# Kernel tuning notes

Hardware: AMD Instinct MI355X
Metric: run time of the kernel (lower is better)

The kernel has to match this reference:

```python
import jax, jax.numpy as jnp
import numpy as np

HIDDEN = 512
LAYERS = 2
MAX_ROLLOUT = 12
STATE_SIZE = [8, 6, 4, 1]
ANCHOR = 64
BATCH = 1024
BLOCK_N = len(STATE_SIZE)


def setup_inputs() -> dict:
    key = jax.random.key(0)
    ks = jax.random.split(key, 20)
    s = 0.05
    d = {}
    d["x0"] = jax.random.normal(ks[0], (1, BATCH, HIDDEN), jnp.float32)
    d["lstm_Wih"] = jax.random.normal(ks[1], (LAYERS, 4 * HIDDEN, HIDDEN), jnp.float32) * s
    d["lstm_Whh"] = jax.random.normal(ks[2], (LAYERS, 4 * HIDDEN, HIDDEN), jnp.float32) * s
    d["lstm_bih"] = jax.random.normal(ks[3], (LAYERS, 4 * HIDDEN), jnp.float32) * s
    d["lstm_bhh"] = jax.random.normal(ks[4], (LAYERS, 4 * HIDDEN), jnp.float32) * s
    d["Wc0"] = jax.random.normal(ks[5], (STATE_SIZE[0], HIDDEN), jnp.float32) * s
    d["bc0"] = jax.random.normal(ks[6], (STATE_SIZE[0],), jnp.float32) * s
    d["Wc1"] = jax.random.normal(ks[7], (STATE_SIZE[1], HIDDEN), jnp.float32) * s
    d["bc1"] = jax.random.normal(ks[8], (STATE_SIZE[1],), jnp.float32) * s
    d["Wc2"] = jax.random.normal(ks[9], (STATE_SIZE[2], HIDDEN), jnp.float32) * s
    d["bc2"] = jax.random.normal(ks[10], (STATE_SIZE[2],), jnp.float32) * s
    d["Wprev"] = jax.random.normal(ks[11], (ANCHOR, HIDDEN), jnp.float32) * s
    d["bprev"] = jax.random.normal(ks[12], (ANCHOR,), jnp.float32) * s
    d["Wcurr"] = jax.random.normal(ks[13], (ANCHOR, HIDDEN), jnp.float32) * s
    d["bcurr"] = jax.random.normal(ks[14], (ANCHOR,), jnp.float32) * s
    d["Wanc"] = jax.random.normal(ks[15], (HIDDEN, MAX_ROLLOUT - 1), jnp.float32) * s
    d["banc"] = jax.random.normal(ks[16], (HIDDEN,), jnp.float32) * s
    d["v"] = jax.random.normal(ks[17], (ANCHOR,), jnp.float32)
    d["batch_size"] = BATCH
    return d


def _lstm_step(x, h, c, Wih, Whh, bih, bhh):
    # x: [B,H]; h,c: [L,B,H]; multi-layer LSTM, torch gate order (i,f,g,o)
    hs, cs = [], []
    inp = x
    for l in range(LAYERS):
        g = inp @ Wih[l].T + h[l] @ Whh[l].T + bih[l] + bhh[l]  # [B,4H]
        gi, gf, gg, go = jnp.split(g, 4, axis=-1)
        cl = jax.nn.sigmoid(gf) * c[l] + jax.nn.sigmoid(gi) * jnp.tanh(gg)
        hl = jax.nn.sigmoid(go) * jnp.tanh(cl)
        hs.append(hl)
        cs.append(cl)
        inp = hl
    return inp, jnp.stack(hs), jnp.stack(cs)


def _forward(x0, lstm_Wih, lstm_Whh, lstm_bih, lstm_bhh, Wc0, bc0, Wc1, bc1, Wc2, bc2,
             Wprev, bprev, Wcurr, bcurr, Wanc, banc, v, batch_size):
    Wcls = [Wc0, Wc1, Wc2]
    bcls = [bc0, bc1, bc2]
    B = batch_size
    anchor_hs = [jnp.zeros((B, HIDDEN), x0.dtype)]
    inp = x0[0]  # [B,H]
    h = jnp.zeros((LAYERS, B, HIDDEN), x0.dtype)
    c = jnp.zeros((LAYERS, B, HIDDEN), x0.dtype)
    outputs = []
    for i in range(MAX_ROLLOUT * BLOCK_N):
        state_idx = i % BLOCK_N
        cycle_idx = i // BLOCK_N
        out, h, c = _lstm_step(inp, h, c, lstm_Wih, lstm_Whh, lstm_bih, lstm_bhh)
        if state_idx < BLOCK_N - 1:
            logit = out @ Wcls[state_idx].T + bcls[state_idx]
            outputs.append(jax.nn.softmax(logit, axis=-1))  # [B, STATE_SIZE[state_idx]]
            # note: `inp` is NOT updated on classifier steps, matching the original
        else:
            anchor_hs.append(out)
            if cycle_idx == 0:
                anchor_o = jnp.zeros((B, MAX_ROLLOUT - 1), x0.dtype)
            else:
                # attention over anchor_hs[0:cycle_idx] (zeros + previous cycles),
                # exactly as the original indexes after appending current out
                prev = jnp.stack(anchor_hs[:cycle_idx])  # [cyc, B, H]
                t = jnp.tanh(prev @ Wprev.T + bprev + (out @ Wcurr.T + bcurr)[None])  # [cyc,B,A]
                scores = jax.nn.sigmoid(jnp.einsum('a,cba->cb', v, t))  # [cyc, B]
                anchor_o = jnp.pad(scores.T, ((0, 0), (0, MAX_ROLLOUT - cycle_idx - 1)))
            outputs.append(anchor_o)  # [B, MAX_ROLLOUT-1]
            inp = anchor_o @ Wanc.T + banc  # anchor_embedding feeds next step
    # outputs are [B, S_i] / [B, MAX_ROLLOUT-1]; concat into a single [B, 348] tensor
    return jnp.concatenate(outputs, axis=1)


def reference(x0, lstm_Wih, lstm_Whh, lstm_bih, lstm_bhh, Wc0, bc0, Wc1, bc1, Wc2, bc2,
              Wprev, bprev, Wcurr, bcurr, Wanc, banc, v, batch_size):
    return _forward(x0, lstm_Wih, lstm_Whh, lstm_bih, lstm_bhh, Wc0, bc0, Wc1, bc1, Wc2, bc2,
                    Wprev, bprev, Wcurr, bcurr, Wanc, banc, v, batch_size)
```

## Files before the change

### kernel.cpp

```cpp
#include <hip/hip_runtime.h>
#include <hip/hip_bf16.h>

#define BATCH 1024
#define HID   512
#define OUTW  348

using short8 = __attribute__((ext_vector_type(8))) short;
using bf16x8 = __attribute__((ext_vector_type(8))) __bf16;
using f32x4  = __attribute__((ext_vector_type(4))) float;

__device__ __forceinline__ float bf2f(unsigned short u) {
  union { unsigned int i; float f; } x; x.i = ((unsigned int)u) << 16; return x.f;
}
__device__ __forceinline__ unsigned short f2bf(float f) {
  __hip_bfloat16 b = __float2bfloat16(f);
  return __builtin_bit_cast(unsigned short, b);
}
__device__ __forceinline__ float sigm(float x) { return 1.0f / (1.0f + __expf(-x)); }

__device__ __forceinline__ f32x4 mfma_bf16(short8 a, short8 b, f32x4 c) {
  return __builtin_amdgcn_mfma_f32_16x16x32_bf16(
      __builtin_bit_cast(bf16x8, a), __builtin_bit_cast(bf16x8, b), c, 0, 0, 0);
}

typedef const __attribute__((address_space(1))) unsigned int* gas_p;
typedef __attribute__((address_space(3))) unsigned int* las_p;
__device__ __forceinline__ void gload16(const void* g, void* l) {
  __builtin_amdgcn_global_load_lds((gas_p)g, (las_p)l, 16, 0, 0);
}


__global__ void k_convert(const float* __restrict__ src, unsigned short* __restrict__ dst, int n) {
  int i = (blockIdx.x * blockDim.x + threadIdx.x) * 4;
  if (i + 3 < n) {
    float4 v = *(const float4*)(src + i);
    dst[i + 0] = f2bf(v.x); dst[i + 1] = f2bf(v.y);
    dst[i + 2] = f2bf(v.z); dst[i + 3] = f2bf(v.w);
  } else {
    for (int j = 0; j < 4 && i + j < n; ++j) dst[i + j] = f2bf(src[i + j]);
  }
}

__global__ void k_wqp(const float* __restrict__ Wcurr, const float* __restrict__ Wprev,
                      unsigned short* __restrict__ dst) {
  int i = blockIdx.x * blockDim.x + threadIdx.x;
  int row = i >> 9, col = i & 511;
  float v = (row < 64) ? Wcurr[row * 512 + col] : Wprev[(row - 64) * 512 + col];
  dst[i] = f2bf(v);
}

__global__ void k_bias(const float* __restrict__ bih, const float* __restrict__ bhh,
                       float* __restrict__ bsum) {
  int i = blockIdx.x * blockDim.x + threadIdx.x;
  if (i < 4096) bsum[i] = bih[i] + bhh[i];
}

__global__ void k_zero(uint4* __restrict__ p, int n16) {
  int i = blockIdx.x * blockDim.x + threadIdx.x;
  if (i < n16) p[i] = make_uint4(0u, 0u, 0u, 0u);
}

__global__ void k_p0(float* __restrict__ P, const float* __restrict__ bprev) {
  int i = blockIdx.x * blockDim.x + threadIdx.x;
  P[i] = bprev[i & 63];
}


struct GJob {
  const unsigned short *X, *H, *Wih, *Whh;
  const float *bias;
  float *C;
  unsigned short *Hout;
};
struct CJob {
  const unsigned short* h;
  const float *Wc, *bc;
  float* out;
  int obase;
};

__device__ __forceinline__ void run_gemm(const GJob& j, int lb,
                                         unsigned short (*Ab)[4096],
                                         unsigned short (*Bb)[4096]) {
  const int w = threadIdx.x >> 6, lane = threadIdx.x & 63;
  const int mt = lb >> 5;
  const int nt = (lb & 7) * 4 + ((lb >> 3) & 3);
  const int m0 = mt * 64;
  const int n0 = nt * 16;
  const int l16 = lane & 15, kg = lane >> 4;

  auto stage = [&](int kt, int buf) {
    const unsigned short* Asrc = (kt < 8) ? j.X : j.H;
    const unsigned short* Wsrc = (kt < 8) ? j.Wih : j.Whh;
    const int k0 = (kt & 7) * 64;
#pragma unroll
    for (int i = 0; i < 2; ++i) {
      int s = w * 128 + i * 64 + lane;
      int row = s >> 3;
      int ke = ((s & 7) ^ (row & 7)) << 3;
      gload16(Asrc + (size_t)(m0 + row) * HID + k0 + ke, &Ab[buf][(w * 128 + i * 64) * 8]);
    }
#pragma unroll
    for (int i = 0; i < 2; ++i) {
      int s = w * 128 + i * 64 + lane;
      int fr = s >> 3;
      int g = fr >> 4, c = fr & 15;
      int ke = ((s & 7) ^ (fr & 7)) << 3;
      gload16(Wsrc + (size_t)(g * 512 + n0 + c) * HID + k0 + ke, &Bb[buf][(w * 128 + i * 64) * 8]);
    }
  };

  f32x4 acc[4];
#pragma unroll
  for (int g = 0; g < 4; ++g) acc[g] = (f32x4)(0.0f);

  stage(0, 0);
  for (int kt = 0; kt < 16; ++kt) {
    __syncthreads();
    if (kt < 15) stage(kt + 1, (kt + 1) & 1);
    const int buf = kt & 1;
#pragma unroll
    for (int ko = 0; ko < 2; ++ko) {
      const int acb = ko * 64 + kg * 16;
      const int ar = w * 16 + l16;
      short8 a = *(const short8*)&Ab[buf][ar * 64 + ((acb ^ ((ar & 7) << 4)) >> 1)];
#pragma unroll
      for (int g = 0; g < 4; ++g) {
        const int br = g * 16 + l16;
        short8 b = *(const short8*)&Bb[buf][br * 64 + ((acb ^ ((br & 7) << 4)) >> 1)];
        acc[g] = mfma_bf16(a, b, acc[g]);
      }
    }
  }

  const int ccol = n0 + l16;
  const int crow = m0 + w * 16 + kg * 4;
  const float b0 = j.bias[ccol], b1 = j.bias[512 + ccol];
  const float b2 = j.bias[1024 + ccol], b3 = j.bias[1536 + ccol];
#pragma unroll
  for (int r = 0; r < 4; ++r) {
    const int m = crow + r;
    float gi = acc[0][r] + b0;
    float gf = acc[1][r] + b1;
    float gg = acc[2][r] + b2;
    float go = acc[3][r] + b3;
    float cold = j.C[m * HID + ccol];
    float cn = sigm(gf) * cold + sigm(gi) * tanhf(gg);
    float hn = sigm(go) * tanhf(cn);
    j.C[m * HID + ccol] = cn;
    j.Hout[m * HID + ccol] = f2bf(hn);
  }
}

template <int S>
__device__ __forceinline__ void run_cls(const CJob& c, int cb) {
  const int w = threadIdx.x >> 6, lane = threadIdx.x & 63;
#pragma unroll
  for (int i = 0; i < 8; ++i) {
    const int r = (cb * 4 + w) * 8 + i;
    short8 hv = *(const short8*)(c.h + r * HID + lane * 8);
    float hf[8];
#pragma unroll
    for (int j = 0; j < 8; ++j) hf[j] = bf2f((unsigned short)hv[j]);
    float logit[S];
#pragma unroll
    for (int s = 0; s < S; ++s) {
      const float* wr = c.Wc + s * HID + lane * 8;
      float p = 0.f;
#pragma unroll
      for (int j = 0; j < 8; ++j) p += hf[j] * wr[j];
#pragma unroll
      for (int off = 32; off; off >>= 1) p += __shfl_xor(p, off);
      logit[s] = p + c.bc[s];
    }
    if (lane == 0) {
      float m = logit[0];
#pragma unroll
      for (int s = 1; s < S; ++s) m = fmaxf(m, logit[s]);
      float e[S], den = 0.f;
#pragma unroll
      for (int s = 0; s < S; ++s) { e[s] = __expf(logit[s] - m); den += e[s]; }
      float inv = 1.0f / den;
#pragma unroll
      for (int s = 0; s < S; ++s) c.out[r * OUTW + c.obase + s] = e[s] * inv;
    }
  }
}

template <int S>
__global__ __launch_bounds__(256, 4) void k_gates1(GJob A, CJob C) {
  __shared__ unsigned short Ab[2][4096];
  __shared__ unsigned short Bb[2][4096];
  const int b = blockIdx.x;
  if (b < 512) {
    run_gemm(A, b, Ab, Bb);
  } else {
    if constexpr (S > 0) run_cls<S>(C, b - 512);
  }
}

__global__ __launch_bounds__(256) void k_qp(
    const unsigned short* __restrict__ h1,
    const unsigned short* __restrict__ Wqp,
    const float* __restrict__ bcurr, const float* __restrict__ bprev,
    float* __restrict__ Q,
    float* __restrict__ P,
    int cyc) {
  __shared__ unsigned short Ab[2][4096];
  __shared__ unsigned short Bb[2][1024];
  const int w = threadIdx.x >> 6, lane = threadIdx.x & 63;
  const int m0 = blockIdx.x * 64, n0 = blockIdx.y * 16;
  const int l16 = lane & 15, kg = lane >> 4;

  auto stage = [&](int kt, int buf) {
    const int k0 = kt * 64;
#pragma unroll
    for (int j = 0; j < 2; ++j) {
      int s = w * 128 + j * 64 + lane;
      int row = s >> 3;
      int ke = ((s & 7) ^ (row & 7)) << 3;
      gload16(h1 + (size_t)(m0 + row) * HID + k0 + ke, &Ab[buf][(w * 128 + j * 64) * 8]);
    }
    if (w < 2) {
      int s = w * 64 + lane;
      int row = s >> 3;
      int ke = ((s & 7) ^ (row & 7)) << 3;
      gload16(Wqp + (size_t)(n0 + row) * HID + k0 + ke, &Bb[buf][(w * 64) * 8]);
    }
  };

  f32x4 acc = (f32x4)(0.0f);
  stage(0, 0);
  for (int kt = 0; kt < 8; ++kt) {
    __syncthreads();
    if (kt < 7) stage(kt + 1, (kt + 1) & 1);
    const int buf = kt & 1;
#pragma unroll
    for (int ko = 0; ko < 2; ++ko) {
      const int acb = ko * 64 + kg * 16;
      const int ar = w * 16 + l16;
      short8 a = *(const short8*)&Ab[buf][ar * 64 + ((acb ^ ((ar & 7) << 4)) >> 1)];
      const int br = l16;
      short8 b = *(const short8*)&Bb[buf][br * 64 + ((acb ^ ((br & 7) << 4)) >> 1)];
      acc = mfma_bf16(a, b, acc);
    }
  }

  const int col = n0 + l16;
  const int r0 = m0 + w * 16 + kg * 4;
#pragma unroll
  for (int r = 0; r < 4; ++r) {
    const int m = r0 + r;
    float val = acc[r] + (col < 64 ? bcurr[col] : bprev[col - 64]);
    if (col < 64) Q[m * 64 + col] = val;
    else if (cyc + 1 < 12) P[(cyc + 1) * (BATCH * 64) + m * 64 + (col - 64)] = val;
  }
}

template <int CYC>
__global__ __launch_bounds__(256) void k_scores(
    const float* __restrict__ Q, const float* __restrict__ P,
    const float* __restrict__ vv, const float* __restrict__ Wanc,
    const float* __restrict__ banc, float* __restrict__ out,
    unsigned short* __restrict__ X) {
  const int w = threadIdx.x >> 6, lane = threadIdx.x & 63;
  const int r = blockIdx.x * 4 + w;
  const float q = Q[r * 64 + lane];
  const float vl = vv[lane];
  float sk[CYC > 0 ? CYC : 1];
#pragma unroll
  for (int k = 0; k < CYC; ++k) {
    float t = tanhf(P[k * (BATCH * 64) + r * 64 + lane] + q) * vl;
#pragma unroll
    for (int off = 32; off; off >>= 1) t += __shfl_xor(t, off);
    sk[k] = sigm(t);
  }
  float ov = 0.0f;
#pragma unroll
  for (int k = 0; k < 11; ++k)
    if (lane == k) ov = (k < CYC) ? sk[k] : 0.0f;
  if (lane < 11) out[r * OUTW + CYC * 29 + 18 + lane] = ov;

  const int d0 = lane * 8;
#pragma unroll
  for (int j = 0; j < 8; ++j) {
    const int d = d0 + j;
    float x = banc[d];
#pragma unroll
    for (int k = 0; k < CYC; ++k) x += sk[k] * Wanc[d * 11 + k];
    X[r * HID + d] = f2bf(x);
  }
}


extern "C" void kernel_launch(void* const* d_in, const int* in_sizes, int n_in,
                              void* d_out, int out_size, void* d_ws, size_t ws_size,
                              hipStream_t stream) {
  const float* x0    = (const float*)d_in[0];
  const float* lWih  = (const float*)d_in[1];
  const float* lWhh  = (const float*)d_in[2];
  const float* lbih  = (const float*)d_in[3];
  const float* lbhh  = (const float*)d_in[4];
  const float* Wc0   = (const float*)d_in[5];
  const float* bc0   = (const float*)d_in[6];
  const float* Wc1   = (const float*)d_in[7];
  const float* bc1   = (const float*)d_in[8];
  const float* Wc2   = (const float*)d_in[9];
  const float* bc2   = (const float*)d_in[10];
  const float* Wprev = (const float*)d_in[11];
  const float* bprev = (const float*)d_in[12];
  const float* Wcurr = (const float*)d_in[13];
  const float* bcurr = (const float*)d_in[14];
  const float* Wanc  = (const float*)d_in[15];
  const float* banc  = (const float*)d_in[16];
  const float* v     = (const float*)d_in[17];
  float* out = (float*)d_out;

  const size_t NW  = 2 * 2048 * 512;
  const size_t NBH = (size_t)BATCH * HID;

  char* ws = (char*)d_ws;
  size_t off = 0;
  auto alloc = [&](size_t bytes) { char* p = ws + off; off += (bytes + 255) & ~(size_t)255; return p; };
  unsigned short* Wih_b = (unsigned short*)alloc(NW * 2);
  unsigned short* Whh_b = (unsigned short*)alloc(NW * 2);
  unsigned short* Wqp_b = (unsigned short*)alloc(128 * 512 * 2);
  float*          biasS = (float*)alloc(4096 * 4);
  unsigned short* Xb    = (unsigned short*)alloc(NBH * 2);
  unsigned short* Hb0   = (unsigned short*)alloc(2 * NBH * 2);
  unsigned short* Hb1   = (unsigned short*)alloc(2 * NBH * 2);
  float*          C0    = (float*)alloc(NBH * 4);
  float*          C1    = (float*)alloc(NBH * 4);
  float*          P     = (float*)alloc((size_t)12 * BATCH * 64 * 4);
  float*          Qb    = (float*)alloc((size_t)BATCH * 64 * 4);

  k_convert<<<dim3((NW / 4 + 255) / 256), dim3(256), 0, stream>>>(lWih, Wih_b, (int)NW);
  k_convert<<<dim3((NW / 4 + 255) / 256), dim3(256), 0, stream>>>(lWhh, Whh_b, (int)NW);
  k_convert<<<dim3((NBH / 4 + 255) / 256), dim3(256), 0, stream>>>(x0, Xb, (int)NBH);
  k_wqp<<<dim3(256), dim3(256), 0, stream>>>(Wcurr, Wprev, Wqp_b);
  k_bias<<<dim3(16), dim3(256), 0, stream>>>(lbih, lbhh, biasS);
  {
    size_t zb = 2 * NBH * 2 + 2 * NBH * 2 + NBH * 4 + NBH * 4;
    int n16 = (int)(zb / 16);
    k_zero<<<dim3((n16 + 255) / 256), dim3(256), 0, stream>>>((uint4*)Hb0, n16);
  }
  k_p0<<<dim3(256), dim3(256), 0, stream>>>(P, bprev);

  auto jobL0 = [&](int u) {
    GJob j; j.X = Xb; j.H = Hb0 + (u & 1) * NBH;
    j.Wih = Wih_b; j.Whh = Whh_b; j.bias = biasS; j.C = C0;
    j.Hout = Hb0 + ((u + 1) & 1) * NBH; return j;
  };
  auto jobL1 = [&](int t) {
    GJob j; j.X = Hb0 + ((t + 1) & 1) * NBH; j.H = Hb1 + (t & 1) * NBH;
    j.Wih = Wih_b + 2048 * 512; j.Whh = Whh_b + 2048 * 512; j.bias = biasS + 2048; j.C = C1;
    j.Hout = Hb1 + ((t + 1) & 1) * NBH; return j;
  };
  auto h1of = [&](int t) { return (const unsigned short*)(Hb1 + ((t + 1) & 1) * NBH); };
  CJob nocls{};

  k_gates1<0><<<dim3(512), dim3(256), 0, stream>>>(jobL0(0), nocls);

  for (int c = 0; c < 12; ++c) {
    const int t0 = 4 * c, t1 = t0 + 1, t2 = t0 + 2, t3 = t0 + 3;
    const int base = c * 29;
    CJob cls0{h1of(t0), Wc0, bc0, out, base};
    CJob cls1{h1of(t1), Wc1, bc1, out, base + 8};
    CJob cls2{h1of(t2), Wc2, bc2, out, base + 14};

    k_gates1<0><<<dim3(512), dim3(256), 0, stream>>>(jobL1(t0), nocls);
    k_gates1<0><<<dim3(512), dim3(256), 0, stream>>>(jobL0(t1), nocls);
    k_gates1<8><<<dim3(544), dim3(256), 0, stream>>>(jobL1(t1), cls0);
    k_gates1<0><<<dim3(512), dim3(256), 0, stream>>>(jobL0(t2), nocls);
    k_gates1<6><<<dim3(544), dim3(256), 0, stream>>>(jobL1(t2), cls1);
    k_gates1<0><<<dim3(512), dim3(256), 0, stream>>>(jobL0(t3), nocls);
    k_gates1<4><<<dim3(544), dim3(256), 0, stream>>>(jobL1(t3), cls2);

    k_qp<<<dim3(16, 8), dim3(256), 0, stream>>>(h1of(t3), Wqp_b, bcurr, bprev, Qb, P, c);
    switch (c) {
      case 0:  k_scores<0><<<dim3(256), dim3(256), 0, stream>>>(Qb, P, v, Wanc, banc, out, Xb); break;
      case 1:  k_scores<1><<<dim3(256), dim3(256), 0, stream>>>(Qb, P, v, Wanc, banc, out, Xb); break;
      case 2:  k_scores<2><<<dim3(256), dim3(256), 0, stream>>>(Qb, P, v, Wanc, banc, out, Xb); break;
      case 3:  k_scores<3><<<dim3(256), dim3(256), 0, stream>>>(Qb, P, v, Wanc, banc, out, Xb); break;
      case 4:  k_scores<4><<<dim3(256), dim3(256), 0, stream>>>(Qb, P, v, Wanc, banc, out, Xb); break;
      case 5:  k_scores<5><<<dim3(256), dim3(256), 0, stream>>>(Qb, P, v, Wanc, banc, out, Xb); break;
      case 6:  k_scores<6><<<dim3(256), dim3(256), 0, stream>>>(Qb, P, v, Wanc, banc, out, Xb); break;
      case 7:  k_scores<7><<<dim3(256), dim3(256), 0, stream>>>(Qb, P, v, Wanc, banc, out, Xb); break;
      case 8:  k_scores<8><<<dim3(256), dim3(256), 0, stream>>>(Qb, P, v, Wanc, banc, out, Xb); break;
      case 9:  k_scores<9><<<dim3(256), dim3(256), 0, stream>>>(Qb, P, v, Wanc, banc, out, Xb); break;
      case 10: k_scores<10><<<dim3(256), dim3(256), 0, stream>>>(Qb, P, v, Wanc, banc, out, Xb); break;
      default: k_scores<11><<<dim3(256), dim3(256), 0, stream>>>(Qb, P, v, Wanc, banc, out, Xb); break;
    }
    if (c < 11)
      k_gates1<0><<<dim3(512), dim3(256), 0, stream>>>(jobL0(t3 + 1), nocls);
  }
  (void)in_sizes; (void)n_in; (void)out_size; (void)ws_size;
}
```

Before: 1.994 ms.

## Halve LSTM GEMM M-tile, interleave gate rows, fuse anchor projection and scoring

The LSTM gate GEMM now uses 32-row M tiles with a 2x2 wave layout and doubles the grid to 1024 blocks. Weight rows are interleaved per cell so that a 16-column MFMA tile holds all four gates, and lane shuffles gather the gates for the cell update. The double-buffer sync is replaced by explicit vmcnt/lgkmcnt waits plus raw barriers. The separate Q/P projection and scoring kernels are fused into one per-16-row kernel that keeps Q in shared memory, which removes a launch and the Q global round trip. The trade-offs are more redundant weight loads per block, shuffle overhead in the epilogue, and only 64 blocks for the fused anchor kernel.

```diff
diff --git a/kernel.cpp b/kernel.cpp
--- a/kernel.cpp
+++ b/kernel.cpp
@@ -80,12 +80,13 @@
 };
 
 __device__ __forceinline__ void run_gemm(const GJob& j, int lb,
-                                         unsigned short (*Ab)[4096],
+                                         unsigned short (*Ab)[2048],
                                          unsigned short (*Bb)[4096]) {
-  const int w = threadIdx.x >> 6, lane = threadIdx.x & 63;
+  const int tid = threadIdx.x, w = tid >> 6, lane = tid & 63;
+  const int wm = w & 1, wn = w >> 1;
   const int mt = lb >> 5;
   const int nt = (lb & 7) * 4 + ((lb >> 3) & 3);
-  const int m0 = mt * 64;
+  const int m0 = mt * 32;
   const int n0 = nt * 16;
   const int l16 = lane & 15, kg = lane >> 4;
 
@@ -93,62 +94,73 @@
     const unsigned short* Asrc = (kt < 8) ? j.X : j.H;
     const unsigned short* Wsrc = (kt < 8) ? j.Wih : j.Whh;
     const int k0 = (kt & 7) * 64;
+    {
+      int s = tid, row = s >> 3;
+      int ke = ((s & 7) ^ (row & 7)) << 3;
+      gload16(Asrc + (size_t)(m0 + row) * HID + k0 + ke, &Ab[buf][s * 8]);
+    }
 #pragma unroll
     for (int i = 0; i < 2; ++i) {
-      int s = w * 128 + i * 64 + lane;
-      int row = s >> 3;
-      int ke = ((s & 7) ^ (row & 7)) << 3;
-      gload16(Asrc + (size_t)(m0 + row) * HID + k0 + ke, &Ab[buf][(w * 128 + i * 64) * 8]);
-    }
-#pragma unroll
-    for (int i = 0; i < 2; ++i) {
-      int s = w * 128 + i * 64 + lane;
-      int fr = s >> 3;
-      int g = fr >> 4, c = fr & 15;
-      int ke = ((s & 7) ^ (fr & 7)) << 3;
-      gload16(Wsrc + (size_t)(g * 512 + n0 + c) * HID + k0 + ke, &Bb[buf][(w * 128 + i * 64) * 8]);
+      int s = i * 256 + tid;
+      int gr = s >> 3;
+      int cell = gr >> 2, g = gr & 3;
+      int ke = ((s & 7) ^ (gr & 7)) << 3;
+      gload16(Wsrc + (size_t)(g * HID + n0 + cell) * HID + k0 + ke, &Bb[buf][s * 8]);
     }
   };
 
-  f32x4 acc[4];
-#pragma unroll
-  for (int g = 0; g < 4; ++g) acc[g] = (f32x4)(0.0f);
+  f32x4 acc[2];
+  acc[0] = (f32x4)(0.0f); acc[1] = (f32x4)(0.0f);
 
   stage(0, 0);
   for (int kt = 0; kt < 16; ++kt) {
-    __syncthreads();
-    if (kt < 15) stage(kt + 1, (kt + 1) & 1);
+    asm volatile("s_waitcnt lgkmcnt(0)" ::: "memory");
+    __builtin_amdgcn_s_barrier();
+    if (kt < 15) {
+      stage(kt + 1, (kt + 1) & 1);
+      asm volatile("s_waitcnt vmcnt(3)" ::: "memory");
+    } else {
+      asm volatile("s_waitcnt vmcnt(0)" ::: "memory");
+    }
+    __builtin_amdgcn_s_barrier();
+    __builtin_amdgcn_sched_barrier(0);
     const int buf = kt & 1;
+    const int ar = wm * 16 + l16;
+    const char* abase = (const char*)&Ab[buf][0] + ar * 128;
+    const char* bbase = (const char*)&Bb[buf][0];
 #pragma unroll
     for (int ko = 0; ko < 2; ++ko) {
-      const int acb = ko * 64 + kg * 16;
-      const int ar = w * 16 + l16;
-      short8 a = *(const short8*)&Ab[buf][ar * 64 + ((acb ^ ((ar & 7) << 4)) >> 1)];
-#pragma unroll
-      for (int g = 0; g < 4; ++g) {
-        const int br = g * 16 + l16;
-        short8 b = *(const short8*)&Bb[buf][br * 64 + ((acb ^ ((br & 7) << 4)) >> 1)];
-        acc[g] = mfma_bf16(a, b, acc[g]);
+      const int kb = ko * 64 + kg * 16;
+      short8 a = *(const short8*)(abase + (kb ^ ((ar & 7) << 4)));
+#pragma unroll
+      for (int t = 0; t < 2; ++t) {
+        const int br = wn * 32 + t * 16 + l16;
+        short8 b = *(const short8*)(bbase + br * 128 + (kb ^ ((br & 7) << 4)));
+        acc[t] = mfma_bf16(a, b, acc[t]);
       }
     }
   }
 
-  const int ccol = n0 + l16;
-  const int crow = m0 + w * 16 + kg * 4;
-  const float b0 = j.bias[ccol], b1 = j.bias[512 + ccol];
-  const float b2 = j.bias[1024 + ccol], b3 = j.bias[1536 + ccol];
-#pragma unroll
-  for (int r = 0; r < 4; ++r) {
-    const int m = crow + r;
-    float gi = acc[0][r] + b0;
-    float gf = acc[1][r] + b1;
-    float gg = acc[2][r] + b2;
-    float go = acc[3][r] + b3;
-    float cold = j.C[m * HID + ccol];
-    float cn = sigm(gf) * cold + sigm(gi) * tanhf(gg);
-    float hn = sigm(go) * tanhf(cn);
-    j.C[m * HID + ccol] = cn;
-    j.Hout[m * HID + ccol] = f2bf(hn);
+  const int g = l16 & 3;
+#pragma unroll
+  for (int t = 0; t < 2; ++t) {
+    const int cell = n0 + wn * 8 + t * 4 + (l16 >> 2);
+    const float bs = j.bias[g * HID + cell];
+#pragma unroll
+    for (int r = 0; r < 4; ++r) {
+      float val = acc[t][r] + bs;
+      float gf = __shfl(val, (lane & ~3) + 1);
+      float gg = __shfl(val, (lane & ~3) + 2);
+      float go = __shfl(val, (lane & ~3) + 3);
+      if (g == 0) {
+        const int m = m0 + wm * 16 + kg * 4 + r;
+        float cold = j.C[m * HID + cell];
+        float cn = sigm(gf) * cold + sigm(val) * tanhf(gg);
+        float hn = sigm(go) * tanhf(cn);
+        j.C[m * HID + cell] = cn;
+        j.Hout[m * HID + cell] = f2bf(hn);
+      }
+    }
   }
 }
 
@@ -189,47 +201,49 @@
 
 template <int S>
 __global__ __launch_bounds__(256, 4) void k_gates1(GJob A, CJob C) {
-  __shared__ unsigned short Ab[2][4096];
+  __shared__ unsigned short Ab[2][2048];
   __shared__ unsigned short Bb[2][4096];
   const int b = blockIdx.x;
-  if (b < 512) {
+  if (b < 1024) {
     run_gemm(A, b, Ab, Bb);
   } else {
-    if constexpr (S > 0) run_cls<S>(C, b - 512);
-  }
-}
-
-__global__ __launch_bounds__(256) void k_qp(
+    if constexpr (S > 0) run_cls<S>(C, b - 1024);
+  }
+}
+
+__global__ __launch_bounds__(256) void k_anchor2(
     const unsigned short* __restrict__ h1,
     const unsigned short* __restrict__ Wqp,
     const float* __restrict__ bcurr, const float* __restrict__ bprev,
-    float* __restrict__ Q,
-    float* __restrict__ P,
-    int cyc) {
-  __shared__ unsigned short Ab[2][4096];
-  __shared__ unsigned short Bb[2][1024];
-  const int w = threadIdx.x >> 6, lane = threadIdx.x & 63;
-  const int m0 = blockIdx.x * 64, n0 = blockIdx.y * 16;
+    const float* __restrict__ vv, const float* __restrict__ Wanc,
+    const float* __restrict__ banc,
+    float* __restrict__ P, float* __restrict__ out,
+    unsigned short* __restrict__ X, int cyc) {
+  __shared__ unsigned short Ab[2][1024];
+  __shared__ unsigned short Bb[2][8192];
+  __shared__ float Qs[16][64];
+  __shared__ float ss[16][12];
+  const int tid = threadIdx.x, w = tid >> 6, lane = tid & 63;
   const int l16 = lane & 15, kg = lane >> 4;
+  const int m0 = blockIdx.x * 16;
 
   auto stage = [&](int kt, int buf) {
     const int k0 = kt * 64;
-#pragma unroll
-    for (int j = 0; j < 2; ++j) {
-      int s = w * 128 + j * 64 + lane;
-      int row = s >> 3;
+    if (tid < 128) {
+      int s = tid, row = s >> 3;
       int ke = ((s & 7) ^ (row & 7)) << 3;
-      gload16(h1 + (size_t)(m0 + row) * HID + k0 + ke, &Ab[buf][(w * 128 + j * 64) * 8]);
-    }
-    if (w < 2) {
-      int s = w * 64 + lane;
-      int row = s >> 3;
+      gload16(h1 + (size_t)(m0 + row) * HID + k0 + ke, &Ab[buf][s * 8]);
+    }
+#pragma unroll
+    for (int i = 0; i < 4; ++i) {
+      int s = i * 256 + tid, row = s >> 3;
       int ke = ((s & 7) ^ (row & 7)) << 3;
-      gload16(Wqp + (size_t)(n0 + row) * HID + k0 + ke, &Bb[buf][(w * 64) * 8]);
+      gload16(Wqp + (size_t)row * HID + k0 + ke, &Bb[buf][s * 8]);
     }
   };
 
-  f32x4 acc = (f32x4)(0.0f);
+  f32x4 acc[2];
+  acc[0] = (f32x4)(0.0f); acc[1] = (f32x4)(0.0f);
   stage(0, 0);
   for (int kt = 0; kt < 8; ++kt) {
     __syncthreads();
@@ -237,58 +251,55 @@
     const int buf = kt & 1;
 #pragma unroll
     for (int ko = 0; ko < 2; ++ko) {
-      const int acb = ko * 64 + kg * 16;
-      const int ar = w * 16 + l16;
-      short8 a = *(const short8*)&Ab[buf][ar * 64 + ((acb ^ ((ar & 7) << 4)) >> 1)];
-      const int br = l16;
-      short8 b = *(const short8*)&Bb[buf][br * 64 + ((acb ^ ((br & 7) << 4)) >> 1)];
-      acc = mfma_bf16(a, b, acc);
-    }
-  }
-
-  const int col = n0 + l16;
-  const int r0 = m0 + w * 16 + kg * 4;
-#pragma unroll
-  for (int r = 0; r < 4; ++r) {
-    const int m = r0 + r;
-    float val = acc[r] + (col < 64 ? bcurr[col] : bprev[col - 64]);
-    if (col < 64) Q[m * 64 + col] = val;
-    else if (cyc + 1 < 12) P[(cyc + 1) * (BATCH * 64) + m * 64 + (col - 64)] = val;
-  }
-}
-
-template <int CYC>
-__global__ __launch_bounds__(256) void k_scores(
-    const float* __restrict__ Q, const float* __restrict__ P,
-    const float* __restrict__ vv, const float* __restrict__ Wanc,
-    const float* __restrict__ banc, float* __restrict__ out,
-    unsigned short* __restrict__ X) {
-  const int w = threadIdx.x >> 6, lane = threadIdx.x & 63;
-  const int r = blockIdx.x * 4 + w;
-  const float q = Q[r * 64 + lane];
-  const float vl = vv[lane];
-  float sk[CYC > 0 ? CYC : 1];
-#pragma unroll
-  for (int k = 0; k < CYC; ++k) {
-    float t = tanhf(P[k * (BATCH * 64) + r * 64 + lane] + q) * vl;
-#pragma unroll
-    for (int off = 32; off; off >>= 1) t += __shfl_xor(t, off);
-    sk[k] = sigm(t);
-  }
-  float ov = 0.0f;
-#pragma unroll
-  for (int k = 0; k < 11; ++k)
-    if (lane == k) ov = (k < CYC) ? sk[k] : 0.0f;
-  if (lane < 11) out[r * OUTW + CYC * 29 + 18 + lane] = ov;
-
-  const int d0 = lane * 8;
-#pragma unroll
-  for (int j = 0; j < 8; ++j) {
-    const int d = d0 + j;
-    float x = banc[d];
-#pragma unroll
-    for (int k = 0; k < CYC; ++k) x += sk[k] * Wanc[d * 11 + k];
-    X[r * HID + d] = f2bf(x);
+      const int kb = ko * 64 + kg * 16;
+      const int ar = l16;
+      short8 a = *(const short8*)((const char*)&Ab[buf][0] + ar * 128 + (kb ^ ((ar & 7) << 4)));
+#pragma unroll
+      for (int t = 0; t < 2; ++t) {
+        const int br = w * 32 + t * 16 + l16;
+        short8 b = *(const short8*)((const char*)&Bb[buf][0] + br * 128 + (kb ^ ((br & 7) << 4)));
+        acc[t] = mfma_bf16(a, b, acc[t]);
+      }
+    }
+  }
+
+#pragma unroll
+  for (int t = 0; t < 2; ++t) {
+    const int col = w * 32 + t * 16 + l16;
+#pragma unroll
+    for (int r = 0; r < 4; ++r) {
+      const int lr = kg * 4 + r;
+      float val = acc[t][r] + (col < 64 ? bcurr[col] : bprev[col - 64]);
+      if (col < 64) Qs[lr][col] = val;
+      else if (cyc + 1 < 12) P[(size_t)(cyc + 1) * (BATCH * 64) + (m0 + lr) * 64 + (col - 64)] = val;
+    }
+  }
+  __syncthreads();
+
+  for (int rr = 0; rr < 4; ++rr) {
+    const int lr = w * 4 + rr;
+    const float q = Qs[lr][lane];
+    float skv = 0.f;
+    for (int k = 0; k < cyc; ++k) {
+      float tt = tanhf(P[(size_t)k * (BATCH * 64) + (m0 + lr) * 64 + lane] + q) * vv[lane];
+#pragma unroll
+      for (int off = 32; off; off >>= 1) tt += __shfl_xor(tt, off);
+      float sk = sigm(tt);
+      if (lane == k) skv = sk;
+      if (lane == 0) ss[lr][k] = sk;
+    }
+    if (lane < 11) out[(size_t)(m0 + lr) * OUTW + cyc * 29 + 18 + lane] = (lane < cyc) ? skv : 0.f;
+  }
+  __syncthreads();
+
+  {
+    const int row = tid >> 4, dseg = tid & 15;
+    for (int jj = 0; jj < 32; ++jj) {
+      const int d = dseg * 32 + jj;
+      float x = banc[d];
+      for (int k = 0; k < cyc; ++k) x += ss[row][k] * Wanc[d * 11 + k];
+      X[(size_t)(m0 + row) * HID + d] = f2bf(x);
+    }
   }
 }
 
@@ -332,7 +343,6 @@
   float*          C0    = (float*)alloc(NBH * 4);
   float*          C1    = (float*)alloc(NBH * 4);
   float*          P     = (float*)alloc((size_t)12 * BATCH * 64 * 4);
-  float*          Qb    = (float*)alloc((size_t)BATCH * 64 * 4);
 
   k_convert<<<dim3((NW / 4 + 255) / 256), dim3(256), 0, stream>>>(lWih, Wih_b, (int)NW);
   k_convert<<<dim3((NW / 4 + 255) / 256), dim3(256), 0, stream>>>(lWhh, Whh_b, (int)NW);
@@ -359,7 +369,7 @@
   auto h1of = [&](int t) { return (const unsigned short*)(Hb1 + ((t + 1) & 1) * NBH); };
   CJob nocls{};
 
-  k_gates1<0><<<dim3(512), dim3(256), 0, stream>>>(jobL0(0), nocls);
+  k_gates1<0><<<dim3(1024), dim3(256), 0, stream>>>(jobL0(0), nocls);
 
   for (int c = 0; c < 12; ++c) {
     const int t0 = 4 * c, t1 = t0 + 1, t2 = t0 + 2, t3 = t0 + 3;
@@ -368,31 +378,18 @@
     CJob cls1{h1of(t1), Wc1, bc1, out, base + 8};
     CJob cls2{h1of(t2), Wc2, bc2, out, base + 14};
 
-    k_gates1<0><<<dim3(512), dim3(256), 0, stream>>>(jobL1(t0), nocls);
-    k_gates1<0><<<dim3(512), dim3(256), 0, stream>>>(jobL0(t1), nocls);
-    k_gates1<8><<<dim3(544), dim3(256), 0, stream>>>(jobL1(t1), cls0);
-    k_gates1<0><<<dim3(512), dim3(256), 0, stream>>>(jobL0(t2), nocls);
-    k_gates1<6><<<dim3(544), dim3(256), 0, stream>>>(jobL1(t2), cls1);
-    k_gates1<0><<<dim3(512), dim3(256), 0, stream>>>(jobL0(t3), nocls);
-    k_gates1<4><<<dim3(544), dim3(256), 0, stream>>>(jobL1(t3), cls2);
-
-    k_qp<<<dim3(16, 8), dim3(256), 0, stream>>>(h1of(t3), Wqp_b, bcurr, bprev, Qb, P, c);
-    switch (c) {
-      case 0:  k_scores<0><<<dim3(256), dim3(256), 0, stream>>>(Qb, P, v, Wanc, banc, out, Xb); break;
-      case 1:  k_scores<1><<<dim3(256), dim3(256), 0, stream>>>(Qb, P, v, Wanc, banc, out, Xb); break;
-      case 2:  k_scores<2><<<dim3(256), dim3(256), 0, stream>>>(Qb, P, v, Wanc, banc, out, Xb); break;
-      case 3:  k_scores<3><<<dim3(256), dim3(256), 0, stream>>>(Qb, P, v, Wanc, banc, out, Xb); break;
-      case 4:  k_scores<4><<<dim3(256), dim3(256), 0, stream>>>(Qb, P, v, Wanc, banc, out, Xb); break;
-      case 5:  k_scores<5><<<dim3(256), dim3(256), 0, stream>>>(Qb, P, v, Wanc, banc, out, Xb); break;
-      case 6:  k_scores<6><<<dim3(256), dim3(256), 0, stream>>>(Qb, P, v, Wanc, banc, out, Xb); break;
-      case 7:  k_scores<7><<<dim3(256), dim3(256), 0, stream>>>(Qb, P, v, Wanc, banc, out, Xb); break;
-      case 8:  k_scores<8><<<dim3(256), dim3(256), 0, stream>>>(Qb, P, v, Wanc, banc, out, Xb); break;
-      case 9:  k_scores<9><<<dim3(256), dim3(256), 0, stream>>>(Qb, P, v, Wanc, banc, out, Xb); break;
-      case 10: k_scores<10><<<dim3(256), dim3(256), 0, stream>>>(Qb, P, v, Wanc, banc, out, Xb); break;
-      default: k_scores<11><<<dim3(256), dim3(256), 0, stream>>>(Qb, P, v, Wanc, banc, out, Xb); break;
-    }
+    k_gates1<0><<<dim3(1024), dim3(256), 0, stream>>>(jobL1(t0), nocls);
+    k_gates1<0><<<dim3(1024), dim3(256), 0, stream>>>(jobL0(t1), nocls);
+    k_gates1<8><<<dim3(1056), dim3(256), 0, stream>>>(jobL1(t1), cls0);
+    k_gates1<0><<<dim3(1024), dim3(256), 0, stream>>>(jobL0(t2), nocls);
+    k_gates1<6><<<dim3(1056), dim3(256), 0, stream>>>(jobL1(t2), cls1);
+    k_gates1<0><<<dim3(1024), dim3(256), 0, stream>>>(jobL0(t3), nocls);
+    k_gates1<4><<<dim3(1056), dim3(256), 0, stream>>>(jobL1(t3), cls2);
+
+    k_anchor2<<<dim3(64), dim3(256), 0, stream>>>(h1of(t3), Wqp_b, bcurr, bprev,
+                                                  v, Wanc, banc, P, out, Xb, c);
     if (c < 11)
-      k_gates1<0><<<dim3(512), dim3(256), 0, stream>>>(jobL0(t3 + 1), nocls);
+      k_gates1<0><<<dim3(1024), dim3(256), 0, stream>>>(jobL0(t3 + 1), nocls);
   }
   (void)in_sizes; (void)n_in; (void)out_size; (void)ws_size;
 }
```

After: 2.298 ms. 15.2% more time.

## Halve gate-GEMM M tile, interleave gates, add triple-buffered async pipeline

Applied to the files above, without the earlier changes.

Shrinks the LSTM gate GEMM tile from 64 rows to 32 rows, doubling the grid to 1024 blocks, and splits the four waves 2x2 over M and N. The B tile now interleaves the four gates per cell, so lane shuffles gather i/f/g/o for the elementwise update. The K loop moves from double to triple buffering with explicit vmcnt waits and raw barriers to overlap loads with MFMA. The aim is more parallelism and better latency hiding for this small-M recurrent GEMM. The cost is fewer MFMAs per byte loaded, extra shuffles, and only a quarter of lanes active in the epilogue.

```diff
diff --git a/kernel.cpp b/kernel.cpp
--- a/kernel.cpp
+++ b/kernel.cpp
@@ -80,12 +80,13 @@
 };
 
 __device__ __forceinline__ void run_gemm(const GJob& j, int lb,
-                                         unsigned short (*Ab)[4096],
+                                         unsigned short (*Ab)[2048],
                                          unsigned short (*Bb)[4096]) {
-  const int w = threadIdx.x >> 6, lane = threadIdx.x & 63;
+  const int tid = threadIdx.x, w = tid >> 6, lane = tid & 63;
+  const int wm = w & 1, wn = w >> 1;
   const int mt = lb >> 5;
   const int nt = (lb & 7) * 4 + ((lb >> 3) & 3);
-  const int m0 = mt * 64;
+  const int m0 = mt * 32;
   const int n0 = nt * 16;
   const int l16 = lane & 15, kg = lane >> 4;
 
@@ -93,62 +94,77 @@
     const unsigned short* Asrc = (kt < 8) ? j.X : j.H;
     const unsigned short* Wsrc = (kt < 8) ? j.Wih : j.Whh;
     const int k0 = (kt & 7) * 64;
+    {
+      int s = tid, row = s >> 3;
+      int ke = ((s & 7) ^ (row & 7)) << 3;
+      gload16(Asrc + (size_t)(m0 + row) * HID + k0 + ke, &Ab[buf][s * 8]);
+    }
 #pragma unroll
     for (int i = 0; i < 2; ++i) {
-      int s = w * 128 + i * 64 + lane;
-      int row = s >> 3;
-      int ke = ((s & 7) ^ (row & 7)) << 3;
-      gload16(Asrc + (size_t)(m0 + row) * HID + k0 + ke, &Ab[buf][(w * 128 + i * 64) * 8]);
-    }
-#pragma unroll
-    for (int i = 0; i < 2; ++i) {
-      int s = w * 128 + i * 64 + lane;
-      int fr = s >> 3;
-      int g = fr >> 4, c = fr & 15;
-      int ke = ((s & 7) ^ (fr & 7)) << 3;
-      gload16(Wsrc + (size_t)(g * 512 + n0 + c) * HID + k0 + ke, &Bb[buf][(w * 128 + i * 64) * 8]);
+      int s = i * 256 + tid;
+      int gr = s >> 3;
+      int cell = gr >> 2, g = gr & 3;
+      int ke = ((s & 7) ^ (gr & 7)) << 3;
+      gload16(Wsrc + (size_t)(g * HID + n0 + cell) * HID + k0 + ke, &Bb[buf][s * 8]);
     }
   };
 
-  f32x4 acc[4];
-#pragma unroll
-  for (int g = 0; g < 4; ++g) acc[g] = (f32x4)(0.0f);
+  f32x4 acc[2];
+  acc[0] = (f32x4)(0.0f); acc[1] = (f32x4)(0.0f);
 
   stage(0, 0);
+  stage(1, 1);
+#pragma unroll
   for (int kt = 0; kt < 16; ++kt) {
-    __syncthreads();
-    if (kt < 15) stage(kt + 1, (kt + 1) & 1);
-    const int buf = kt & 1;
+    asm volatile("s_waitcnt lgkmcnt(0)" ::: "memory");
+    __builtin_amdgcn_s_barrier();
+    if (kt <= 13) {
+      stage(kt + 2, (kt + 2) % 3);
+      asm volatile("s_waitcnt vmcnt(6)" ::: "memory");
+    } else if (kt == 14) {
+      asm volatile("s_waitcnt vmcnt(3)" ::: "memory");
+    } else {
+      asm volatile("s_waitcnt vmcnt(0)" ::: "memory");
+    }
+    __builtin_amdgcn_s_barrier();
+    __builtin_amdgcn_sched_barrier(0);
+    const int buf = kt % 3;
+    const int ar = wm * 16 + l16;
+    const char* abase = (const char*)&Ab[buf][0] + ar * 128;
+    const char* bbase = (const char*)&Bb[buf][0];
 #pragma unroll
     for (int ko = 0; ko < 2; ++ko) {
-      const int acb = ko * 64 + kg * 16;
-      const int ar = w * 16 + l16;
-      short8 a = *(const short8*)&Ab[buf][ar * 64 + ((acb ^ ((ar & 7) << 4)) >> 1)];
-#pragma unroll
-      for (int g = 0; g < 4; ++g) {
-        const int br = g * 16 + l16;
-        short8 b = *(const short8*)&Bb[buf][br * 64 + ((acb ^ ((br & 7) << 4)) >> 1)];
-        acc[g] = mfma_bf16(a, b, acc[g]);
+      const int kb = ko * 64 + kg * 16;
+      short8 a = *(const short8*)(abase + (kb ^ ((ar & 7) << 4)));
+#pragma unroll
+      for (int t = 0; t < 2; ++t) {
+        const int br = wn * 32 + t * 16 + l16;
+        short8 b = *(const short8*)(bbase + br * 128 + (kb ^ ((br & 7) << 4)));
+        acc[t] = mfma_bf16(a, b, acc[t]);
       }
     }
   }
 
-  const int ccol = n0 + l16;
-  const int crow = m0 + w * 16 + kg * 4;
-  const float b0 = j.bias[ccol], b1 = j.bias[512 + ccol];
-  const float b2 = j.bias[1024 + ccol], b3 = j.bias[1536 + ccol];
-#pragma unroll
-  for (int r = 0; r < 4; ++r) {
-    const int m = crow + r;
-    float gi = acc[0][r] + b0;
-    float gf = acc[1][r] + b1;
-    float gg = acc[2][r] + b2;
-    float go = acc[3][r] + b3;
-    float cold = j.C[m * HID + ccol];
-    float cn = sigm(gf) * cold + sigm(gi) * tanhf(gg);
-    float hn = sigm(go) * tanhf(cn);
-    j.C[m * HID + ccol] = cn;
-    j.Hout[m * HID + ccol] = f2bf(hn);
+  const int g = l16 & 3;
+#pragma unroll
+  for (int t = 0; t < 2; ++t) {
+    const int cell = n0 + wn * 8 + t * 4 + (l16 >> 2);
+    const float bs = j.bias[g * HID + cell];
+#pragma unroll
+    for (int r = 0; r < 4; ++r) {
+      float val = acc[t][r] + bs;
+      float gf = __shfl(val, (lane & ~3) + 1);
+      float gg = __shfl(val, (lane & ~3) + 2);
+      float go = __shfl(val, (lane & ~3) + 3);
+      if (g == 0) {
+        const int m = m0 + wm * 16 + kg * 4 + r;
+        float cold = j.C[m * HID + cell];
+        float cn = sigm(gf) * cold + sigm(val) * tanhf(gg);
+        float hn = sigm(go) * tanhf(cn);
+        j.C[m * HID + cell] = cn;
+        j.Hout[m * HID + cell] = f2bf(hn);
+      }
+    }
   }
 }
 
@@ -189,13 +205,13 @@
 
 template <int S>
 __global__ __launch_bounds__(256, 4) void k_gates1(GJob A, CJob C) {
-  __shared__ unsigned short Ab[2][4096];
-  __shared__ unsigned short Bb[2][4096];
+  __shared__ unsigned short Ab[3][2048];
+  __shared__ unsigned short Bb[3][4096];
   const int b = blockIdx.x;
-  if (b < 512) {
+  if (b < 1024) {
     run_gemm(A, b, Ab, Bb);
   } else {
-    if constexpr (S > 0) run_cls<S>(C, b - 512);
+    if constexpr (S > 0) run_cls<S>(C, b - 1024);
   }
 }
 
@@ -359,7 +375,7 @@
   auto h1of = [&](int t) { return (const unsigned short*)(Hb1 + ((t + 1) & 1) * NBH); };
   CJob nocls{};
 
-  k_gates1<0><<<dim3(512), dim3(256), 0, stream>>>(jobL0(0), nocls);
+  k_gates1<0><<<dim3(1024), dim3(256), 0, stream>>>(jobL0(0), nocls);
 
   for (int c = 0; c < 12; ++c) {
     const int t0 = 4 * c, t1 = t0 + 1, t2 = t0 + 2, t3 = t0 + 3;
@@ -368,13 +384,13 @@
     CJob cls1{h1of(t1), Wc1, bc1, out, base + 8};
     CJob cls2{h1of(t2), Wc2, bc2, out, base + 14};
 
-    k_gates1<0><<<dim3(512), dim3(256), 0, stream>>>(jobL1(t0), nocls);
-    k_gates1<0><<<dim3(512), dim3(256), 0, stream>>>(jobL0(t1), nocls);
-    k_gates1<8><<<dim3(544), dim3(256), 0, stream>>>(jobL1(t1), cls0);
-    k_gates1<0><<<dim3(512), dim3(256), 0, stream>>>(jobL0(t2), nocls);
-    k_gates1<6><<<dim3(544), dim3(256), 0, stream>>>(jobL1(t2), cls1);
-    k_gates1<0><<<dim3(512), dim3(256), 0, stream>>>(jobL0(t3), nocls);
-    k_gates1<4><<<dim3(544), dim3(256), 0, stream>>>(jobL1(t3), cls2);
+    k_gates1<0><<<dim3(1024), dim3(256), 0, stream>>>(jobL1(t0), nocls);
+    k_gates1<0><<<dim3(1024), dim3(256), 0, stream>>>(jobL0(t1), nocls);
+    k_gates1<8><<<dim3(1056), dim3(256), 0, stream>>>(jobL1(t1), cls0);
+    k_gates1<0><<<dim3(1024), dim3(256), 0, stream>>>(jobL0(t2), nocls);
+    k_gates1<6><<<dim3(1056), dim3(256), 0, stream>>>(jobL1(t2), cls1);
+    k_gates1<0><<<dim3(1024), dim3(256), 0, stream>>>(jobL0(t3), nocls);
+    k_gates1<4><<<dim3(1056), dim3(256), 0, stream>>>(jobL1(t3), cls2);
 
     k_qp<<<dim3(16, 8), dim3(256), 0, stream>>>(h1of(t3), Wqp_b, bcurr, bprev, Qb, P, c);
     switch (c) {
@@ -392,7 +408,7 @@
       default: k_scores<11><<<dim3(256), dim3(256), 0, stream>>>(Qb, P, v, Wanc, banc, out, Xb); break;
     }
     if (c < 11)
-      k_gates1<0><<<dim3(512), dim3(256), 0, stream>>>(jobL0(t3 + 1), nocls);
+      k_gates1<0><<<dim3(1024), dim3(256), 0, stream>>>(jobL0(t3 + 1), nocls);
   }
   (void)in_sizes; (void)n_in; (void)out_size; (void)ws_size;
 }
```

New measurement: 2.177 ms. +9.2%, slower.
